# Performance work log

Hardware: AMD Instinct MI355X
Metric: run time of the kernel (lower is better)

Reference implementation:

```python
import jax, jax.numpy as jnp
import numpy as np

# Unpooled output spatial size (pooled 128x128 -> unpooled 256x256)
OUT_H, OUT_W = 256, 256


def setup_inputs() -> dict:
    key = jax.random.key(0)
    k1, k2, k3, k4 = jax.random.split(key, 4)
    B, C, OH, OW = 16, 64, 128, 128
    K, P = 4, 4  # kernel_size samples, bilinear taps
    x = jax.random.normal(k1, (B, C, OH, OW), dtype=jnp.float32)
    idx_mask = jax.random.randint(k2, (B, C, OH, OW), 0, K, dtype=jnp.int64)
    sample_map = jax.random.randint(k3, (OH, OW, K, P), 0, OUT_H * OUT_W, dtype=jnp.int64)
    interp_weights = jax.random.uniform(k4, (OH, OW, K, P), dtype=jnp.float32)
    return {"x": x, "idx_mask": idx_mask, "sample_map": sample_map,
            "interp_weights": interp_weights}


def reference(x, idx_mask, sample_map, interp_weights):
    # x: (B,C,OH,OW) pooled values; idx_mask: (B,C,OH,OW) argmax kernel sample in [0,K)
    # sample_map: (OH,OW,K,P) flat indices into OUT_H*OUT_W; interp_weights: (OH,OW,K,P)
    B, C, OH, OW = x.shape
    P = sample_map.shape[-1]
    oh = jnp.arange(OH)[:, None]
    ow = jnp.arange(OW)[None, :]
    # Select, per (b,c,oh,ow), the winning kernel sample's taps and weights -> (B,C,OH,OW,P)
    sel_idx = sample_map[oh, ow, idx_mask]
    sel_w = interp_weights[oh, ow, idx_mask]
    vals = sel_w * x[..., None]  # (B,C,OH,OW,P)
    bb = jnp.arange(B)[:, None, None, None, None]
    cc = jnp.arange(C)[None, :, None, None, None]
    out = jnp.zeros((B, C, OUT_H * OUT_W), dtype=x.dtype)
    out = out.at[bb, cc, sel_idx].add(vals)  # scatter-add (atomic add in CUDA kernel)
    return out.reshape(B, C, OUT_H, OUT_W)
```

## Files before the change

### kernel.cpp

```cpp
#include <hip/hip_runtime.h>
#include <hip/hip_fp16.h>

constexpr int B  = 16;
constexpr int C  = 64;
constexpr int OH = 128;
constexpr int OW = 128;
constexpr int HW = OH * OW;
constexpr int K  = 4;
constexpr int P  = 4;
constexpr int TAPS = HW * K * P;
constexpr int OUT_H = 256;
constexpr int OUT_W = 256;
constexpr int PLANE = OUT_H * OUT_W;
constexpr int NQ = 4;
constexpr int QUARTER = PLANE / NQ;
constexpr int BLOCK = 512;
constexpr size_t TABLE_BYTES = (size_t)HW * K * 16;

constexpr int CHUNK_CAP = 114688;
constexpr size_t WS_CHUNK_BYTES = ((size_t)PLANE * 3) * 4 + (size_t)CHUNK_CAP * 16;

static __device__ __forceinline__ float h2f(unsigned short u) {
    __half h; __builtin_memcpy(&h, &u, 2); return __half2float(h);
}


__global__ __launch_bounds__(256) void zero_ws_kernel(
    unsigned* __restrict__ counts, uint4* __restrict__ entries)
{
    int r = blockIdx.x * 256 + threadIdx.x;
    if (r < PLANE)     counts[r]  = 0u;
    if (r < CHUNK_CAP) entries[r] = make_uint4(0u, 0u, 0u, 0u);
}

__global__ __launch_bounds__(256) void hist_kernel(
    const int* __restrict__ sm, unsigned* __restrict__ counts)
{
    int r = blockIdx.x * 256 + threadIdx.x;
    if (r < TAPS) atomicAdd(&counts[sm[r]], 1u);
}

__global__ __launch_bounds__(1024) void scan_chunks_kernel(
    const unsigned* __restrict__ counts,
    unsigned* __restrict__ desc, unsigned* __restrict__ cursor)
{
    __shared__ unsigned part[1024];
    const int t = threadIdx.x;
    const int base = t * 64;
    unsigned s = 0;
    for (int j = 0; j < 64; ++j) s += (counts[base + j] + 3u) >> 2;
    part[t] = s;
    __syncthreads();
    for (int st = 1; st < 1024; st <<= 1) {
        unsigned v = (t >= st) ? part[t - st] : 0u;
        __syncthreads();
        part[t] += v;
        __syncthreads();
    }
    unsigned run = part[t] - s;
    for (int j = 0; j < 64; ++j) {
        unsigned c   = counts[base + j];
        unsigned nch = (c + 3u) >> 2;
        desc[base + j]   = run | (nch << 24);
        cursor[base + j] = run * 4u;
        run += nch;
    }
}

__global__ __launch_bounds__(256) void scatter_chunks_kernel(
    const int* __restrict__ sm, const float* __restrict__ iw,
    unsigned* __restrict__ cursor, unsigned* __restrict__ entries_u32)
{
    int r = blockIdx.x * 256 + threadIdx.x;
    if (r >= TAPS) return;
    int o = sm[r];
    unsigned hw = (unsigned)(r >> 4);
    unsigned k  = (unsigned)((r >> 2) & 3);
    __half h = __float2half_rn(iw[r]);
    unsigned short hb; __builtin_memcpy(&hb, &h, 2);
    unsigned ent = (hw << 2) | k | ((unsigned)hb << 16);
    unsigned pos = atomicAdd(&cursor[o], 1u);
    entries_u32[pos] = ent;
}

__global__ __launch_bounds__(1024, 8) void unpool_chunk_kernel(
    const float* __restrict__ x,
    const int*   __restrict__ idx_mask,
    const unsigned* __restrict__ desc,
    const uint4* __restrict__ entries,
    float* __restrict__ out)
{
    __shared__ unsigned xk[HW];

    const int bc = blockIdx.x;
    const float4* xp4 = (const float4*)(x + (size_t)bc * HW);
    const int4*   ip4 = (const int4*)(idx_mask + (size_t)bc * HW);
    uint4* xk4 = (uint4*)xk;

    for (int t = threadIdx.x; t < HW / 4; t += 1024) {
        float4 xv = xp4[t];
        int4   kv = ip4[t];
        uint4 o;
        o.x = (__float_as_uint(xv.x) & ~3u) | ((unsigned)kv.x & 3u);
        o.y = (__float_as_uint(xv.y) & ~3u) | ((unsigned)kv.y & 3u);
        o.z = (__float_as_uint(xv.z) & ~3u) | ((unsigned)kv.z & 3u);
        o.w = (__float_as_uint(xv.w) & ~3u) | ((unsigned)kv.w & 3u);
        xk4[t] = o;
    }
    __syncthreads();

    const char* xkb = (const char*)xk;
    float* op = out + (size_t)bc * PLANE;

    for (int i = 0; i < PLANE / 1024; ++i) {
        const int o = i * 1024 + threadIdx.x;
        const unsigned d   = desc[o];
        const unsigned nch = d >> 24;
        const uint4* ep = entries + (d & 0xffffffu);
        float acc = 0.f;
        for (unsigned j = 0; j < nch; ++j) {
            uint4 ch = ep[j];
            {   unsigned e = ch.x;
                unsigned u = *(const unsigned*)(xkb + (e & 0xfffcu));
                float w = (((u ^ e) & 3u) == 0u) ? h2f((unsigned short)(e >> 16)) : 0.f;
                acc = fmaf(w, __uint_as_float(u & ~3u), acc); }
            {   unsigned e = ch.y;
                unsigned u = *(const unsigned*)(xkb + (e & 0xfffcu));
                float w = (((u ^ e) & 3u) == 0u) ? h2f((unsigned short)(e >> 16)) : 0.f;
                acc = fmaf(w, __uint_as_float(u & ~3u), acc); }
            {   unsigned e = ch.z;
                unsigned u = *(const unsigned*)(xkb + (e & 0xfffcu));
                float w = (((u ^ e) & 3u) == 0u) ? h2f((unsigned short)(e >> 16)) : 0.f;
                acc = fmaf(w, __uint_as_float(u & ~3u), acc); }
            {   unsigned e = ch.w;
                unsigned u = *(const unsigned*)(xkb + (e & 0xfffcu));
                float w = (((u ^ e) & 3u) == 0u) ? h2f((unsigned short)(e >> 16)) : 0.f;
                acc = fmaf(w, __uint_as_float(u & ~3u), acc); }
        }
        op[o] = acc;
    }
}


static __device__ __forceinline__ uint4 sel4(bool c, uint4 a, uint4 b) {
    return make_uint4(c ? a.x : b.x, c ? a.y : b.y, c ? a.z : b.z, c ? a.w : b.w);
}
static __device__ __forceinline__ float2 u2f2(unsigned u) {
    __half2 h; __builtin_memcpy(&h, &u, 4); return __half22float2(h);
}

__global__ __launch_bounds__(256) void compact_table_kernel(
    const int4* __restrict__ sm, const float4* __restrict__ iw, uint4* __restrict__ ct)
{
    int r = blockIdx.x * blockDim.x + threadIdx.x;
    if (r >= HW * K) return;
    int4   s = sm[r];
    float4 w = iw[r];
    uint4 o;
    o.x = ((unsigned)s.x & 0xffffu) | (((unsigned)s.y & 0xffffu) << 16);
    o.y = ((unsigned)s.z & 0xffffu) | (((unsigned)s.w & 0xffffu) << 16);
    __half2 h01 = __floats2half2_rn(w.x, w.y);
    __half2 h23 = __floats2half2_rn(w.z, w.w);
    __builtin_memcpy(&o.z, &h01, 4);
    __builtin_memcpy(&o.w, &h23, 4);
    ct[r] = o;
}

__global__ __launch_bounds__(BLOCK) void unpool_lds2_kernel(
    const float* __restrict__ x,
    const int*   __restrict__ idx_mask,
    const uint4* __restrict__ ct,
    float* __restrict__ out)
{
    __shared__ float acc[QUARTER];

    const int bc    = blockIdx.x >> 2;
    const int q     = blockIdx.x & 3;
    const int qbase = q * QUARTER;

    float4* acc4 = (float4*)acc;
    for (int t = threadIdx.x; t < QUARTER / 4; t += BLOCK)
        acc4[t] = make_float4(0.f, 0.f, 0.f, 0.f);
    __syncthreads();

    const float* xp = x + (size_t)bc * HW;
    const int*   ip = idx_mask + (size_t)bc * HW;

    for (int hw = threadIdx.x; hw < HW; hw += BLOCK) {
        float xv = xp[hw];
        int   k  = ip[hw];
        const uint4* c = ct + (hw << 2);
        uint4 r0 = c[0], r1 = c[1], r2 = c[2], r3 = c[3];
        uint4 rl = sel4(k & 1, r1, r0);
        uint4 rh = sel4(k & 1, r3, r2);
        uint4 r  = sel4(k & 2, rh, rl);

        int i0 = r.x & 0xffff, i1 = (int)(r.x >> 16);
        int i2 = r.y & 0xffff, i3 = (int)(r.y >> 16);
        float2 w01 = u2f2(r.z);
        float2 w23 = u2f2(r.w);

        int a;
        a = i0 - qbase; if ((unsigned)a < (unsigned)QUARTER) atomicAdd(&acc[a], w01.x * xv);
        a = i1 - qbase; if ((unsigned)a < (unsigned)QUARTER) atomicAdd(&acc[a], w01.y * xv);
        a = i2 - qbase; if ((unsigned)a < (unsigned)QUARTER) atomicAdd(&acc[a], w23.x * xv);
        a = i3 - qbase; if ((unsigned)a < (unsigned)QUARTER) atomicAdd(&acc[a], w23.y * xv);
    }
    __syncthreads();

    float4* op4 = (float4*)(out + (size_t)bc * PLANE + qbase);
    for (int t = threadIdx.x; t < QUARTER / 4; t += BLOCK)
        op4[t] = acc4[t];
}

__global__ __launch_bounds__(256) void unpool_lds_fallback_kernel(
    const float* __restrict__ x,
    const int*   __restrict__ idx_mask,
    const int4*  __restrict__ sample_map,
    const float4* __restrict__ interp_w,
    float* __restrict__ out)
{
    __shared__ float acc[QUARTER];
    const int bc    = blockIdx.x >> 2;
    const int q     = blockIdx.x & 3;
    const int qbase = q * QUARTER;
    float4* acc4 = (float4*)acc;
    for (int t = threadIdx.x; t < QUARTER / 4; t += 256)
        acc4[t] = make_float4(0.f, 0.f, 0.f, 0.f);
    __syncthreads();
    const float* xp = x + (size_t)bc * HW;
    const int*   ip = idx_mask + (size_t)bc * HW;
    for (int hw = threadIdx.x; hw < HW; hw += 256) {
        float xv = xp[hw];
        int   k  = ip[hw];
        int row = hw * K + k;
        int4   sel = sample_map[row];
        float4 w   = interp_w[row];
        int a;
        a = sel.x - qbase; if ((unsigned)a < (unsigned)QUARTER) atomicAdd(&acc[a], w.x * xv);
        a = sel.y - qbase; if ((unsigned)a < (unsigned)QUARTER) atomicAdd(&acc[a], w.y * xv);
        a = sel.z - qbase; if ((unsigned)a < (unsigned)QUARTER) atomicAdd(&acc[a], w.z * xv);
        a = sel.w - qbase; if ((unsigned)a < (unsigned)QUARTER) atomicAdd(&acc[a], w.w * xv);
    }
    __syncthreads();
    float4* op4 = (float4*)(out + (size_t)bc * PLANE + qbase);
    for (int t = threadIdx.x; t < QUARTER / 4; t += 256)
        op4[t] = acc4[t];
}

extern "C" void kernel_launch(void* const* d_in, const int* in_sizes, int n_in,
                              void* d_out, int out_size, void* d_ws, size_t ws_size,
                              hipStream_t stream) {
    const float*  x          = (const float*)d_in[0];
    const int*    idx_mask   = (const int*)d_in[1];
    const int*    sample_map = (const int*)d_in[2];
    const float*  interp_w   = (const float*)d_in[3];
    float* out = (float*)d_out;

    if (ws_size >= WS_CHUNK_BYTES) {
        unsigned* desc    = (unsigned*)d_ws;
        unsigned* cursor  = desc + PLANE;
        unsigned* counts  = cursor + PLANE;
        uint4*    entries = (uint4*)(counts + PLANE);

        zero_ws_kernel<<<(CHUNK_CAP + 255) / 256, 256, 0, stream>>>(counts, entries);
        hist_kernel<<<TAPS / 256, 256, 0, stream>>>(sample_map, counts);
        scan_chunks_kernel<<<1, 1024, 0, stream>>>(counts, desc, cursor);
        scatter_chunks_kernel<<<TAPS / 256, 256, 0, stream>>>(
            sample_map, interp_w, cursor, (unsigned*)entries);
        unpool_chunk_kernel<<<B * C, 1024, 0, stream>>>(x, idx_mask, desc, entries, out);
    } else if (ws_size >= TABLE_BYTES) {
        uint4* ct = (uint4*)d_ws;
        compact_table_kernel<<<(HW * K + 255) / 256, 256, 0, stream>>>(
            (const int4*)sample_map, (const float4*)interp_w, ct);
        unpool_lds2_kernel<<<B * C * NQ, BLOCK, 0, stream>>>(
            x, idx_mask, ct, out);
    } else {
        unpool_lds_fallback_kernel<<<B * C * NQ, 256, 0, stream>>>(
            x, idx_mask, (const int4*)sample_map, (const float4*)interp_w, out);
    }
}
```

Measured before the change: 571.2 us.

## Sort output pixels by chunk count to balance per-thread work in gather kernel

Adds a single-block counting sort that orders output positions by their number of tap chunks and emits a (descriptor, output index) schedule. The gather kernel then reads this schedule, so threads in a wavefront handle outputs with similar loop trip counts, which reduces divergence. In exchange, output stores become scattered instead of coalesced, the per-output metadata read doubles in size, and an extra serial single-block kernel runs each call. The workspace requirement grows by two planes.

```diff
diff --git a/kernel.cpp b/kernel.cpp
--- a/kernel.cpp
+++ b/kernel.cpp
@@ -18,7 +18,7 @@
 constexpr size_t TABLE_BYTES = (size_t)HW * K * 16;
 
 constexpr int CHUNK_CAP = 114688;
-constexpr size_t WS_CHUNK_BYTES = ((size_t)PLANE * 3) * 4 + (size_t)CHUNK_CAP * 16;
+constexpr size_t WS_SORT_BYTES = ((size_t)PLANE * 5) * 4 + (size_t)CHUNK_CAP * 16;
 
 static __device__ __forceinline__ float h2f(unsigned short u) {
     __half h; __builtin_memcpy(&h, &u, 2); return __half2float(h);
@@ -83,10 +83,72 @@
     entries_u32[pos] = ent;
 }
 
-__global__ __launch_bounds__(1024, 8) void unpool_chunk_kernel(
+constexpr int NB  = 32;
+constexpr int ST  = 512;
+constexpr int SPT = PLANE / ST;
+__global__ __launch_bounds__(ST) void sort_outputs_kernel(
+    const unsigned* __restrict__ desc, uint2* __restrict__ sched)
+{
+    __shared__ unsigned short lh[NB][ST];
+    __shared__ unsigned part2[16][NB];
+    __shared__ unsigned bin_base[NB];
+    const int t = threadIdx.x;
+
+    for (int b = 0; b < NB; ++b) lh[b][t] = 0;
+    __syncthreads();
+
+    const int obase = t * SPT;
+    for (int j = 0; j < SPT; ++j) {
+        unsigned nch = desc[obase + j] >> 24;
+        if (nch > 31u) nch = 31u;
+        lh[nch][t]++;
+    }
+    __syncthreads();
+
+    {
+        int b = t & 31, seg = t >> 5;
+        unsigned s = 0;
+        for (int r = 0; r < 32; ++r) s += lh[b][seg * 32 + r];
+        part2[seg][b] = s;
+    }
+    __syncthreads();
+    if (t < NB) {
+        unsigned run = 0;
+        for (int seg = 0; seg < 16; ++seg) {
+            unsigned v = part2[seg][t]; part2[seg][t] = run; run += v;
+        }
+        bin_base[t] = run;
+    }
+    __syncthreads();
+    if (t == 0) {
+        unsigned run = 0;
+        for (int b = 0; b < NB; ++b) { unsigned v = bin_base[b]; bin_base[b] = run; run += v; }
+    }
+    __syncthreads();
+    {
+        int b = t & 31, seg = t >> 5;
+        unsigned run = bin_base[b] + part2[seg][b];
+        for (int r = 0; r < 32; ++r) {
+            int row = seg * 32 + r;
+            unsigned v = lh[b][row];
+            lh[b][row] = (unsigned short)run;
+            run += v;
+        }
+    }
+    __syncthreads();
+    for (int j = 0; j < SPT; ++j) {
+        unsigned d   = desc[obase + j];
+        unsigned nch = d >> 24; if (nch > 31u) nch = 31u;
+        unsigned p = lh[nch][t];
+        lh[nch][t] = (unsigned short)(p + 1u);
+        sched[p] = make_uint2(d, (unsigned)(obase + j));
+    }
+}
+
+__global__ __launch_bounds__(1024, 8) void unpool_sorted_kernel(
     const float* __restrict__ x,
     const int*   __restrict__ idx_mask,
-    const unsigned* __restrict__ desc,
+    const uint2* __restrict__ sched,
     const uint4* __restrict__ entries,
     float* __restrict__ out)
 {
@@ -113,10 +175,9 @@
     float* op = out + (size_t)bc * PLANE;
 
     for (int i = 0; i < PLANE / 1024; ++i) {
-        const int o = i * 1024 + threadIdx.x;
-        const unsigned d   = desc[o];
-        const unsigned nch = d >> 24;
-        const uint4* ep = entries + (d & 0xffffffu);
+        const uint2 s = sched[i * 1024 + threadIdx.x];
+        const unsigned nch = s.x >> 24;
+        const uint4* ep = entries + (s.x & 0xffffffu);
         float acc = 0.f;
         for (unsigned j = 0; j < nch; ++j) {
             uint4 ch = ep[j];
@@ -137,7 +198,7 @@
                 float w = (((u ^ e) & 3u) == 0u) ? h2f((unsigned short)(e >> 16)) : 0.f;
                 acc = fmaf(w, __uint_as_float(u & ~3u), acc); }
         }
-        op[o] = acc;
+        op[s.y] = acc;
     }
 }
 
@@ -257,18 +318,20 @@
     const float*  interp_w   = (const float*)d_in[3];
     float* out = (float*)d_out;
 
-    if (ws_size >= WS_CHUNK_BYTES) {
+    if (ws_size >= WS_SORT_BYTES) {
         unsigned* desc    = (unsigned*)d_ws;
         unsigned* cursor  = desc + PLANE;
         unsigned* counts  = cursor + PLANE;
-        uint4*    entries = (uint4*)(counts + PLANE);
+        uint2*    sched   = (uint2*)(counts + PLANE);
+        uint4*    entries = (uint4*)(counts + PLANE + 2 * PLANE);
 
         zero_ws_kernel<<<(CHUNK_CAP + 255) / 256, 256, 0, stream>>>(counts, entries);
         hist_kernel<<<TAPS / 256, 256, 0, stream>>>(sample_map, counts);
         scan_chunks_kernel<<<1, 1024, 0, stream>>>(counts, desc, cursor);
         scatter_chunks_kernel<<<TAPS / 256, 256, 0, stream>>>(
             sample_map, interp_w, cursor, (unsigned*)entries);
-        unpool_chunk_kernel<<<B * C, 1024, 0, stream>>>(x, idx_mask, desc, entries, out);
+        sort_outputs_kernel<<<1, ST, 0, stream>>>(desc, sched);
+        unpool_sorted_kernel<<<B * C, 1024, 0, stream>>>(x, idx_mask, sched, entries, out);
     } else if (ws_size >= TABLE_BYTES) {
         uint4* ct = (uint4*)d_ws;
         compact_table_kernel<<<(HW * K + 255) / 256, 256, 0, stream>>>(
```

New measurement: 677.9 us. 18.7% more time.
